# Kernel optimization log

Hardware: AMD Instinct MI355X
Metric: run time of the kernel (lower is better)

## Reference

```python
import jax, jax.numpy as jnp
import numpy as np

N = 384
C = 128     # pair_dim
H = 4       # num_head
D = C // H  # key/value dim per head = 32
LN_EPS = 1e-5


def setup_inputs() -> dict:
    key = jax.random.key(0)
    ks = jax.random.split(key, 12)
    s = 1.0 / np.sqrt(C)
    return {
        "pair_act": jax.random.normal(ks[0], (N, N, C), jnp.float32),
        "pair_mask": jax.random.randint(ks[1], (N, N), 0, 2, jnp.int32),
        "ln_scale": jax.random.uniform(ks[2], (C,), jnp.float32),
        "ln_bias": jax.random.normal(ks[3], (C,), jnp.float32) * 0.1,
        "feat_2d_weights": jax.random.normal(ks[4], (C, H), jnp.float32) * s,
        "q_w": jax.random.normal(ks[5], (C, H, D), jnp.float32) * s,
        "k_w": jax.random.normal(ks[6], (C, H, D), jnp.float32) * s,
        "v_w": jax.random.normal(ks[7], (C, H, D), jnp.float32) * s,
        "gating_w": jax.random.normal(ks[8], (C, H, D), jnp.float32) * s,
        "gating_b": jax.random.normal(ks[9], (H, D), jnp.float32) * 0.1,
        "o_w": jax.random.normal(ks[10], (H, D, C), jnp.float32) * s,
        "o_b": jax.random.normal(ks[11], (C,), jnp.float32) * 0.1,
    }


def reference(pair_act, pair_mask, ln_scale, ln_bias, feat_2d_weights,
              q_w, k_w, v_w, gating_w, gating_b, o_w, o_b):
    # orientation == 'per_row': no transpose
    # mask bias: [B, 1, 1, K]
    bias = (1e9 * (pair_mask.astype(pair_act.dtype) - 1.0))[:, None, None, :]
    # query_norm (LayerNorm over last dim)
    mu = jnp.mean(pair_act, axis=-1, keepdims=True)
    var = jnp.mean(jnp.square(pair_act - mu), axis=-1, keepdims=True)
    x = (pair_act - mu) * jax.lax.rsqrt(var + LN_EPS) * ln_scale + ln_bias
    # nonbatched pairwise bias per head: [H, Q, K]
    nb_bias = jnp.einsum('qkc,ch->hqk', x, feat_2d_weights)
    # AF2 gated attention (q_data = m_data = x)
    q = jnp.einsum('bqc,chd->bqhd', x, q_w) * (D ** -0.5)
    k = jnp.einsum('bkc,chd->bkhd', x, k_w)
    v = jnp.einsum('bkc,chd->bkhd', x, v_w)
    logits = jnp.einsum('bqhd,bkhd->bhqk', q, k) + bias + nb_bias[None]
    weights = jax.nn.softmax(logits, axis=-1)
    wavg = jnp.einsum('bhqk,bkhd->bqhd', weights, v)
    gate = jax.nn.sigmoid(jnp.einsum('bqc,chd->bqhd', x, gating_w) + gating_b)
    wavg = wavg * gate
    out = jnp.einsum('bqhd,hdc->bqc', wavg, o_w) + o_b
    return out
```

## Files before the change

### kernel.cpp

```cpp
#include <hip/hip_runtime.h>

typedef __bf16 bf16;
typedef __bf16 bf16x8 __attribute__((ext_vector_type(8)));
typedef __bf16 bf16x4v __attribute__((ext_vector_type(4)));
typedef short s16x4 __attribute__((ext_vector_type(4)));
typedef float f32x4 __attribute__((ext_vector_type(4)));
typedef unsigned int u32;
typedef unsigned long long u64;

#define NN 384
#define CC 128
#define LOG2E 1.44269504088896f

#define MFMA16(a,b,c) __builtin_amdgcn_mfma_f32_16x16x32_bf16(a,b,c,0,0,0)

#if __has_builtin(__builtin_amdgcn_mfma_f32_16x16x16_bf16)
typedef bf16x4v pvab_t;
static __device__ __forceinline__ f32x4 PVMFMA(pvab_t A, bf16x4v B, f32x4 C){
  return __builtin_amdgcn_mfma_f32_16x16x16_bf16(A, B, C, 0,0,0);
}
static __device__ __forceinline__ pvab_t mk_pvab(u32 w0, u32 w1){
  return __builtin_bit_cast(pvab_t, (u64)w0 | ((u64)w1<<32));
}
#else
typedef s16x4 pvab_t;
static __device__ __forceinline__ f32x4 PVMFMA(pvab_t A, bf16x4v B, f32x4 C){
  return __builtin_amdgcn_mfma_f32_16x16x16bf16_1k(A, __builtin_bit_cast(s16x4, B), C, 0,0,0);
}
static __device__ __forceinline__ pvab_t mk_pvab(u32 w0, u32 w1){
  return __builtin_bit_cast(pvab_t, (u64)w0 | ((u64)w1<<32));
}
#endif

static __device__ __forceinline__ u32 bpack(float a, float b){
  unsigned short x = __builtin_bit_cast(unsigned short, (bf16)a);
  unsigned short y = __builtin_bit_cast(unsigned short, (bf16)b);
  return (u32)x | ((u32)y<<16);
}

#define WS_NB   37748736
#define WS_QKVG 40108032
#define WS_OP   40239104
#define WS_KB   40271872
#define WS_VB   78020608
#define WS_NEED 115769344

__device__ __forceinline__ void async_copy16(void* lds_dst, const void* gsrc){
  __builtin_amdgcn_global_load_lds((const __attribute__((address_space(1))) u32*)gsrc,
                                   (__attribute__((address_space(3))) u32*)lds_dst, 16, 0, 0);
}

__global__ __launch_bounds__(256) void pack_kernel(
    const float* __restrict__ qw, const float* __restrict__ kw,
    const float* __restrict__ vw, const float* __restrict__ gw,
    const float* __restrict__ ow, bf16* __restrict__ qkvg, bf16* __restrict__ op)
{
  int tid = blockIdx.x*256 + threadIdx.x;
  int lane = tid & 63, frag = tid >> 6;
  if (frag < 128) {
    int f = frag & 1, t = (frag>>1)&3, h = (frag>>3)&3, wm = frag>>5;
    const float* W = wm==0?qw: (wm==1?kw: (wm==2?vw: gw));
    float sc = (wm==0) ? 0.17677669529663687f*LOG2E : (wm==3 ? LOG2E : 1.0f);
    int d = f*16 + (lane&15);
    #pragma unroll
    for (int j=0;j<8;j++){
      int c = t*32 + (lane>>4)*8 + j;
      qkvg[tid*8 + j] = (bf16)(W[c*128 + h*32 + d]*sc);
    }
  } else if (frag < 160) {
    int fr = frag - 128, f = fr & 7, t = fr>>3;
    int c = f*16 + (lane&15);
    #pragma unroll
    for (int j=0;j<8;j++){
      int d = (lane>>4)*8 + j;
      op[(fr*64 + lane)*8 + j] = (bf16)ow[(t*32 + d)*128 + c];
    }
  }
}

__global__ __launch_bounds__(256) void ln_kernel(
    const float* __restrict__ pa, const float* __restrict__ lns,
    const float* __restrict__ lnb, const float* __restrict__ fw,
    bf16* __restrict__ xout, float* __restrict__ nbout)
{
  int wid = (blockIdx.x*256 + threadIdx.x) >> 6;
  int lane = threadIdx.x & 63;
  int nw = (gridDim.x*256) >> 6;
  float2 sc = *(const float2*)(lns + lane*2);
  float2 bi = *(const float2*)(lnb + lane*2);
  float4 f0 = *(const float4*)(fw + lane*8);
  float4 f1 = *(const float4*)(fw + lane*8 + 4);
  for (int row = wid; row < NN*NN; row += nw){
    float2 v = *(const float2*)(pa + row*128 + lane*2);
    float s = v.x + v.y;
    float sq = v.x*v.x + v.y*v.y;
    #pragma unroll
    for (int m=1;m<64;m<<=1){ s += __shfl_xor(s,m); sq += __shfl_xor(sq,m); }
    float mu = s*(1.f/128.f);
    float rstd = rsqrtf(sq*(1.f/128.f) - mu*mu + 1e-5f);
    float x0 = (v.x-mu)*rstd*sc.x + bi.x;
    float x1 = (v.y-mu)*rstd*sc.y + bi.y;
    unsigned short h0 = __builtin_bit_cast(unsigned short, (bf16)x0);
    unsigned short h1 = __builtin_bit_cast(unsigned short, (bf16)x1);
    *(unsigned int*)((char*)xout + row*256 + lane*4) = ((unsigned int)h1<<16)|h0;
    float4 t;
    t.x = x0*f0.x + x1*f1.x;
    t.y = x0*f0.y + x1*f1.y;
    t.z = x0*f0.z + x1*f1.z;
    t.w = x0*f0.w + x1*f1.w;
    #pragma unroll
    for (int m=1;m<64;m<<=1){
      t.x += __shfl_xor(t.x,m); t.y += __shfl_xor(t.y,m);
      t.z += __shfl_xor(t.z,m); t.w += __shfl_xor(t.w,m);
    }
    float vsel = (lane==0)?t.x : (lane==1)?t.y : (lane==2)?t.z : t.w;
    if (lane < 4) nbout[(size_t)lane*(NN*NN) + row] = vsel*LOG2E;
  }
}

__global__ __launch_bounds__(256) void proj_kv_kernel(
    const bf16* __restrict__ xg, const bf16* __restrict__ qkvg,
    const int* __restrict__ mask, bf16* __restrict__ kbuf, bf16* __restrict__ vbuf)
{
  __shared__ char psm[16384];
  const int w = threadIdx.x>>6, lane = threadIdx.x&63, g = (lane>>4)&3, l15 = lane&15;
  const int W = blockIdx.x*4 + w;
  const int rt = W>>1, wm = 1 + (W&1);
  const f32x4 Z = {0.f,0.f,0.f,0.f};
  f32x4 acc[8];
  #pragma unroll
  for (int f8=0;f8<8;f8++) acc[f8] = Z;
  const bf16* xrow = xg + (size_t)(rt*16 + l15)*CC;
  #pragma unroll
  for (int t=0;t<4;t++){
    bf16x8 a = *(const bf16x8*)(xrow + t*32 + g*8);
    #pragma unroll
    for (int f8=0; f8<8; f8++){
      int h = f8>>1, fh = f8&1;
      bf16x8 bb = *(const bf16x8*)(qkvg + (((wm*4+h)*4+t)*2+fh)*512 + lane*8);
      acc[f8] = MFMA16(a, bb, acc[f8]);
    }
  }
  const int bq = rt/24, tau = rt%24;
  if (wm==1){
    char* scr = psm + w*4096;
    #pragma unroll
    for (int f8=0; f8<8; f8++){
      #pragma unroll
      for (int j=0;j<4;j++){
        unsigned r = g*4+j;
        *(bf16*)(scr + ((r*256 + (f8*16+l15)*2) ^ (((r>>1)&7)<<4))) = (bf16)acc[f8][j];
      }
    }
    #pragma unroll
    for (int h=0;h<4;h++){
      bf16x8 kf = *(const bf16x8*)(scr + ((l15*256 + h*64 + g*16) ^ (((l15>>1)&7)<<4)));
      *(bf16x8*)(kbuf + (((size_t)(bq*4+h)*24 + tau)*64 + lane)*8) = kf;
    }
  } else {
    int4 mi = *(const int4*)(mask + bq*NN + tau*16 + g*4);
    float mb[4] = { mi.x?1.f:0.f, mi.y?1.f:0.f, mi.z?1.f:0.f, mi.w?1.f:0.f };
    #pragma unroll
    for (int f8=0; f8<8; f8++){
      #pragma unroll
      for (int j=0;j<4;j++) acc[f8][j] *= mb[j];
    }
    #pragma unroll
    for (int h=0;h<4;h++){
      f32x4 a0 = acc[h*2+0], a1 = acc[h*2+1];
      uint4 st4;
      st4.x = bpack(a0[0], a0[1]);
      st4.y = bpack(a0[2], a0[3]);
      st4.z = bpack(a1[0], a1[1]);
      st4.w = bpack(a1[2], a1[3]);
      *(uint4*)((char*)vbuf + ((size_t)(bq*4+h)*24 + tau)*1024 + lane*16) = st4;
    }
  }
}

#define L14_SCR  49152
#define L14_MASK 53248
#define L14_TOT  54016

__global__ __attribute__((amdgpu_flat_work_group_size(256,256), amdgpu_waves_per_eu(2,4)))
void attn_kernel14(
    const bf16* __restrict__ xg, const int* __restrict__ mask,
    const float* __restrict__ nb, const bf16* __restrict__ qkvg,
    bf16* __restrict__ kbuf, const bf16* __restrict__ vbuf,
    const float* __restrict__ gb)
{
  __shared__ char sm[L14_TOT];
  const int tid = threadIdx.x;
  const int lane = tid & 63, w = tid >> 6;
  const int g = (lane >> 4)&3, l15 = lane & 15;
  const f32x4 Z = {0.f,0.f,0.f,0.f};

  const u32 bid = blockIdx.x;
  const int h = bid / 384;
  const int b = bid - h*384;

  const char* kbh = (const char*)kbuf + ((size_t)b*4 + h)*24576;
  const char* vbh = (const char*)vbuf + ((size_t)b*4 + h)*24576;

  #pragma unroll
  for (int i=0;i<6;i++){
    unsigned u = (i*4 + w)*1024;
    async_copy16(sm + u,         kbh + u + lane*16);
    async_copy16(sm + 24576 + u, vbh + u + lane*16);
  }
  for (int k = tid; k < NN; k += 256)
    *(bf16*)(sm + L14_MASK + k*2) = (bf16)(float)(mask[b*NN + k] != 0);
  __syncthreads();

  const unsigned scb = L14_SCR + w*1024;
  const float* nbh = nb + (size_t)h*(NN*NN);

  for (int i=0;i<6;i++){
    const int qt = w*6 + i;
    const int qb = qt*16;

    bf16x8 a4[4];
    #pragma unroll
    for (int t=0;t<4;t++)
      a4[t] = *(const bf16x8*)(xg + (size_t)(b*NN + qb + l15)*CC + t*32 + g*8);

    f32x4 q0=Z, q1=Z;
    #pragma unroll
    for (int t=0;t<4;t++){
      bf16x8 bq0 = *(const bf16x8*)(qkvg + (((0*4+h)*4+t)*2+0)*512 + lane*8);
      bf16x8 bq1 = *(const bf16x8*)(qkvg + (((0*4+h)*4+t)*2+1)*512 + lane*8);
      q0 = MFMA16(a4[t], bq0, q0);
      q1 = MFMA16(a4[t], bq1, q1);
    }
    #pragma unroll
    for (int f=0;f<2;f++){
      f32x4 qq = f ? q1 : q0;
      #pragma unroll
      for (int j=0;j<4;j++){
        unsigned r = g*4 + j, cb = (f*16 + l15)*2;
        *(bf16*)(sm + scb + ((r*64 + cb) ^ (((r>>1)&7)<<4))) = (bf16)qq[j];
      }
    }
    bf16x8 aq = *(const bf16x8*)(sm + scb + ((l15*64 + g*16) ^ (((l15>>1)&7)<<4)));

    f32x4 o0=Z, o1=Z, o2=Z;
    const float* nbq = nbh + (size_t)(qb + l15)*NN;

    #pragma unroll
    for (int c=0;c<6;c++){
      f32x4 st[4];
      #pragma unroll
      for (int nf=0;nf<4;nf++){
        float4 nbv = *(const float4*)(nbq + c*64 + nf*16 + g*4);
        bf16x8 ka = *(const bf16x8*)(sm + (c*4+nf)*1024 + lane*16);
        st[nf] = MFMA16(ka, aq, __builtin_bit_cast(f32x4, nbv));
      }
      #pragma unroll
      for (int nf=0;nf<4;nf++){
        #pragma unroll
        for (int j=0;j<4;j++)
          st[nf][j] = exp2f(st[nf][j] - 28.8539008178f);
      }
      #pragma unroll
      for (int nf=0;nf<4;nf++){
        pvab_t pa = mk_pvab(bpack(st[nf][0], st[nf][1]), bpack(st[nf][2], st[nf][3]));
        bf16x4v mk4 = *(const bf16x4v*)(sm + L14_MASK + (c*64 + nf*16 + g*4)*2);
        bf16x8 vv = *(const bf16x8*)(sm + 24576 + (c*4+nf)*1024 + lane*16);
        bf16x4v vlo = {vv[0],vv[1],vv[2],vv[3]};
        bf16x4v vhi = {vv[4],vv[5],vv[6],vv[7]};
        o0 = PVMFMA(pa, vlo, o0);
        o1 = PVMFMA(pa, vhi, o1);
        o2 = PVMFMA(pa, mk4, o2);
      }
    }

    float rcd[4];
    #pragma unroll
    for (int j=0;j<4;j++)
      rcd[j] = __builtin_amdgcn_rcpf(o2[j]);

    f32x4 g0=Z, g1=Z;
    #pragma unroll
    for (int t=0;t<4;t++){
      bf16x8 bg0 = *(const bf16x8*)(qkvg + (((3*4+h)*4+t)*2+0)*512 + lane*8);
      bf16x8 bg1 = *(const bf16x8*)(qkvg + (((3*4+h)*4+t)*2+1)*512 + lane*8);
      g0 = MFMA16(a4[t], bg0, g0);
      g1 = MFMA16(a4[t], bg1, g1);
    }

    #pragma unroll
    for (int f=0;f<2;f++){
      f32x4 ov = f ? o1 : o0, gv = f ? g1 : g0;
      int d = f*16 + l15;
      float gbv = gb[h*32 + d]*LOG2E;
      #pragma unroll
      for (int j=0;j<4;j++){
        float gt = 1.f/(1.f + exp2f(-(gv[j] + gbv)));
        float wg = ov[j]*rcd[j]*gt;
        unsigned r = g*4 + j, cb2 = (unsigned)d*2;
        *(bf16*)(sm + scb + ((r*64 + cb2) ^ (((r>>1)&7)<<4))) = (bf16)wg;
      }
    }
    bf16x8 awg = *(const bf16x8*)(sm + scb + ((l15*64 + g*16) ^ (((l15>>1)&7)<<4)));
    *(bf16x8*)((char*)kbuf + ((size_t)b*4 + h)*24576 + qt*1024 + lane*16) = awg;
  }
}

__global__ __launch_bounds__(256) void outproj_kernel(
    const bf16* __restrict__ wavg, const bf16* __restrict__ opk,
    const float* __restrict__ ob, float* __restrict__ out)
{
  const int w = threadIdx.x>>6, lane = threadIdx.x&63;
  const int g = (lane>>4)&3, l15 = lane&15;
  const f32x4 Z = {0.f,0.f,0.f,0.f};
  const int W = blockIdx.x*4 + w;
  const int b = W/24, qt = W%24, qb = qt*16;

  bf16x8 aw[4];
  #pragma unroll
  for (int h=0;h<4;h++)
    aw[h] = *(const bf16x8*)((const char*)wavg + ((size_t)b*4 + h)*24576 + qt*1024 + lane*16);

  f32x4 outa[8];
  #pragma unroll
  for (int nf=0;nf<8;nf++) outa[nf] = Z;
  #pragma unroll
  for (int h=0;h<4;h++){
    #pragma unroll
    for (int nf=0;nf<8;nf++){
      bf16x8 bo = *(const bf16x8*)(opk + ((h*8+nf)*64 + lane)*8);
      outa[nf] = MFMA16(aw[h], bo, outa[nf]);
    }
  }
  #pragma unroll
  for (int nf=0;nf<8;nf++){
    int c = nf*16 + l15;
    float obv = ob[c];
    #pragma unroll
    for (int j=0;j<4;j++){
      int qi = qb + g*4 + j;
      out[((size_t)b*NN + qi)*CC + c] = outa[nf][j] + obv;
    }
  }
}

extern "C" void kernel_launch(void* const* d_in, const int* in_sizes, int n_in,
                              void* d_out, int out_size, void* d_ws, size_t ws_size,
                              hipStream_t stream)
{
  (void)in_sizes; (void)n_in; (void)out_size; (void)ws_size;
  const float* pa  = (const float*)d_in[0];
  const int*   msk = (const int*)d_in[1];
  const float* lns = (const float*)d_in[2];
  const float* lnb = (const float*)d_in[3];
  const float* fw  = (const float*)d_in[4];
  const float* qw  = (const float*)d_in[5];
  const float* kw  = (const float*)d_in[6];
  const float* vw  = (const float*)d_in[7];
  const float* gw  = (const float*)d_in[8];
  const float* gbv = (const float*)d_in[9];
  const float* ow  = (const float*)d_in[10];
  const float* ob  = (const float*)d_in[11];
  float* out = (float*)d_out;

  char* ws = (char*)d_ws;
  bf16*  xbuf  = (bf16*)(ws);
  float* nbbuf = (float*)(ws + WS_NB);
  bf16*  qkvg  = (bf16*)(ws + WS_QKVG);
  bf16*  opk   = (bf16*)(ws + WS_OP);
  bf16*  kbuf  = (bf16*)(ws + WS_KB);
  bf16*  vbuf  = (bf16*)(ws + WS_VB);

  pack_kernel<<<40, 256, 0, stream>>>(qw, kw, vw, gw, ow, qkvg, opk);
  ln_kernel<<<1152, 256, 0, stream>>>(pa, lns, lnb, fw, xbuf, nbbuf);
  proj_kv_kernel<<<4608, 256, 0, stream>>>(xbuf, qkvg, msk, kbuf, vbuf);
  attn_kernel14<<<1536, 256, 0, stream>>>(xbuf, msk, nbbuf, qkvg, kbuf, vbuf, gbv);
  outproj_kernel<<<2304, 256, 0, stream>>>(kbuf, opk, ob, out);
}
```

Baseline: 322.7 us.

## Compute Q transposed in registers, use 16x16x16 QK MFMAs, move mask into exponent

The Q projection is computed transposed (weights as the A operand), so its output fragment feeds a pair of 16x16x16 MFMAs directly. This removes the LDS scratch write/read round trip for Q, and the K buffer layout is split into two halves to match. The mask becomes an additive -1e9*log2e bias inside the exponent, and the softmax denominator is a register sum with cross-lane shuffles instead of an extra mask MFMA. This trades one MFMA per tile for scalar adds and shuffles, and the QK step now issues twice as many smaller MFMAs.

```diff
diff --git a/kernel.cpp b/kernel.cpp
--- a/kernel.cpp
+++ b/kernel.cpp
@@ -19,18 +19,18 @@
 static __device__ __forceinline__ f32x4 PVMFMA(pvab_t A, bf16x4v B, f32x4 C){
   return __builtin_amdgcn_mfma_f32_16x16x16_bf16(A, B, C, 0,0,0);
 }
-static __device__ __forceinline__ pvab_t mk_pvab(u32 w0, u32 w1){
-  return __builtin_bit_cast(pvab_t, (u64)w0 | ((u64)w1<<32));
-}
 #else
 typedef s16x4 pvab_t;
 static __device__ __forceinline__ f32x4 PVMFMA(pvab_t A, bf16x4v B, f32x4 C){
   return __builtin_amdgcn_mfma_f32_16x16x16bf16_1k(A, __builtin_bit_cast(s16x4, B), C, 0,0,0);
 }
+#endif
 static __device__ __forceinline__ pvab_t mk_pvab(u32 w0, u32 w1){
   return __builtin_bit_cast(pvab_t, (u64)w0 | ((u64)w1<<32));
 }
-#endif
+static __device__ __forceinline__ pvab_t as_pvab(bf16x4v v){
+  return __builtin_bit_cast(pvab_t, v);
+}
 
 static __device__ __forceinline__ u32 bpack(float a, float b){
   unsigned short x = __builtin_bit_cast(unsigned short, (bf16)a);
@@ -154,8 +154,11 @@
     }
     #pragma unroll
     for (int h=0;h<4;h++){
-      bf16x8 kf = *(const bf16x8*)(scr + ((l15*256 + h*64 + g*16) ^ (((l15>>1)&7)<<4)));
-      *(bf16x8*)(kbuf + (((size_t)(bq*4+h)*24 + tau)*64 + lane)*8) = kf;
+      bf16x4v k0 = *(const bf16x4v*)(scr + ((l15*256 + h*64      + g*8) ^ (((l15>>1)&7)<<4)));
+      bf16x4v k1 = *(const bf16x4v*)(scr + ((l15*256 + h*64 + 32 + g*8) ^ (((l15>>1)&7)<<4)));
+      char* base = (char*)kbuf + (((size_t)(bq*4+h)*24 + tau)*1024);
+      *(bf16x4v*)(base +       lane*8) = k0;
+      *(bf16x4v*)(base + 512 + lane*8) = k1;
     }
   } else {
     int4 mi = *(const int4*)(mask + bq*NN + tau*16 + g*4);
@@ -178,18 +181,18 @@
   }
 }
 
-#define L14_SCR  49152
-#define L14_MASK 53248
-#define L14_TOT  54016
+#define L17_SCR  49152
+#define L17_MASK 53248
+#define L17_TOT  54016
 
 __global__ __attribute__((amdgpu_flat_work_group_size(256,256), amdgpu_waves_per_eu(2,4)))
-void attn_kernel14(
+void attn_kernel17(
     const bf16* __restrict__ xg, const int* __restrict__ mask,
     const float* __restrict__ nb, const bf16* __restrict__ qkvg,
     bf16* __restrict__ kbuf, const bf16* __restrict__ vbuf,
     const float* __restrict__ gb)
 {
-  __shared__ char sm[L14_TOT];
+  __shared__ char sm[L17_TOT];
   const int tid = threadIdx.x;
   const int lane = tid & 63, w = tid >> 6;
   const int g = (lane >> 4)&3, l15 = lane & 15;
@@ -209,10 +212,10 @@
     async_copy16(sm + 24576 + u, vbh + u + lane*16);
   }
   for (int k = tid; k < NN; k += 256)
-    *(bf16*)(sm + L14_MASK + k*2) = (bf16)(float)(mask[b*NN + k] != 0);
+    *(bf16*)(sm + L17_MASK + k*2) = (bf16)(1.44269504e9f*((float)mask[b*NN + k] - 1.0f));
   __syncthreads();
 
-  const unsigned scb = L14_SCR + w*1024;
+  const unsigned scb = L17_SCR + w*1024;
   const float* nbh = nb + (size_t)h*(NN*NN);
 
   for (int i=0;i<6;i++){
@@ -224,26 +227,19 @@
     for (int t=0;t<4;t++)
       a4[t] = *(const bf16x8*)(xg + (size_t)(b*NN + qb + l15)*CC + t*32 + g*8);
 
-    f32x4 q0=Z, q1=Z;
+    f32x4 Qt0=Z, Qt1=Z;
     #pragma unroll
     for (int t=0;t<4;t++){
-      bf16x8 bq0 = *(const bf16x8*)(qkvg + (((0*4+h)*4+t)*2+0)*512 + lane*8);
-      bf16x8 bq1 = *(const bf16x8*)(qkvg + (((0*4+h)*4+t)*2+1)*512 + lane*8);
-      q0 = MFMA16(a4[t], bq0, q0);
-      q1 = MFMA16(a4[t], bq1, q1);
-    }
-    #pragma unroll
-    for (int f=0;f<2;f++){
-      f32x4 qq = f ? q1 : q0;
-      #pragma unroll
-      for (int j=0;j<4;j++){
-        unsigned r = g*4 + j, cb = (f*16 + l15)*2;
-        *(bf16*)(sm + scb + ((r*64 + cb) ^ (((r>>1)&7)<<4))) = (bf16)qq[j];
-      }
-    }
-    bf16x8 aq = *(const bf16x8*)(sm + scb + ((l15*64 + g*16) ^ (((l15>>1)&7)<<4)));
-
-    f32x4 o0=Z, o1=Z, o2=Z;
+      bf16x8 wq0 = *(const bf16x8*)(qkvg + (((0*4+h)*4+t)*2+0)*512 + lane*8);
+      bf16x8 wq1 = *(const bf16x8*)(qkvg + (((0*4+h)*4+t)*2+1)*512 + lane*8);
+      Qt0 = MFMA16(wq0, a4[t], Qt0);
+      Qt1 = MFMA16(wq1, a4[t], Qt1);
+    }
+    bf16x4v qb0 = {(bf16)Qt0[0], (bf16)Qt0[1], (bf16)Qt0[2], (bf16)Qt0[3]};
+    bf16x4v qb1 = {(bf16)Qt1[0], (bf16)Qt1[1], (bf16)Qt1[2], (bf16)Qt1[3]};
+
+    float sum_ = 0.f;
+    f32x4 o0=Z, o1=Z;
     const float* nbq = nbh + (size_t)(qb + l15)*NN;
 
     #pragma unroll
@@ -252,32 +248,39 @@
       #pragma unroll
       for (int nf=0;nf<4;nf++){
         float4 nbv = *(const float4*)(nbq + c*64 + nf*16 + g*4);
-        bf16x8 ka = *(const bf16x8*)(sm + (c*4+nf)*1024 + lane*16);
-        st[nf] = MFMA16(ka, aq, __builtin_bit_cast(f32x4, nbv));
+        bf16x4v kA0 = *(const bf16x4v*)(sm + (c*4+nf)*1024 +       lane*8);
+        bf16x4v kA1 = *(const bf16x4v*)(sm + (c*4+nf)*1024 + 512 + lane*8);
+        f32x4 s0 = PVMFMA(as_pvab(kA0), qb0, __builtin_bit_cast(f32x4, nbv));
+        st[nf]   = PVMFMA(as_pvab(kA1), qb1, s0);
       }
       #pragma unroll
       for (int nf=0;nf<4;nf++){
+        bf16x4v mk4 = *(const bf16x4v*)(sm + L17_MASK + (c*64 + nf*16 + g*4)*2);
         #pragma unroll
-        for (int j=0;j<4;j++)
-          st[nf][j] = exp2f(st[nf][j] - 28.8539008178f);
+        for (int j=0;j<4;j++){
+          float pv = exp2f(st[nf][j] + (float)mk4[j] - 28.8539008178f);
+          st[nf][j] = pv;
+          sum_ += pv;
+        }
       }
       #pragma unroll
       for (int nf=0;nf<4;nf++){
         pvab_t pa = mk_pvab(bpack(st[nf][0], st[nf][1]), bpack(st[nf][2], st[nf][3]));
-        bf16x4v mk4 = *(const bf16x4v*)(sm + L14_MASK + (c*64 + nf*16 + g*4)*2);
         bf16x8 vv = *(const bf16x8*)(sm + 24576 + (c*4+nf)*1024 + lane*16);
         bf16x4v vlo = {vv[0],vv[1],vv[2],vv[3]};
         bf16x4v vhi = {vv[4],vv[5],vv[6],vv[7]};
         o0 = PVMFMA(pa, vlo, o0);
         o1 = PVMFMA(pa, vhi, o1);
-        o2 = PVMFMA(pa, mk4, o2);
-      }
-    }
-
+      }
+    }
+
+    sum_ += __shfl_xor(sum_, 16);
+    sum_ += __shfl_xor(sum_, 32);
+    float rsl = 1.f/sum_;
     float rcd[4];
     #pragma unroll
     for (int j=0;j<4;j++)
-      rcd[j] = __builtin_amdgcn_rcpf(o2[j]);
+      rcd[j] = __shfl(rsl, (lane & 0x30) + g*4 + j);
 
     f32x4 g0=Z, g1=Z;
     #pragma unroll
@@ -374,6 +377,6 @@
   pack_kernel<<<40, 256, 0, stream>>>(qw, kw, vw, gw, ow, qkvg, opk);
   ln_kernel<<<1152, 256, 0, stream>>>(pa, lns, lnb, fw, xbuf, nbbuf);
   proj_kv_kernel<<<4608, 256, 0, stream>>>(xbuf, qkvg, msk, kbuf, vbuf);
-  attn_kernel14<<<1536, 256, 0, stream>>>(xbuf, msk, nbbuf, qkvg, kbuf, vbuf, gbv);
+  attn_kernel17<<<1536, 256, 0, stream>>>(xbuf, msk, nbbuf, qkvg, kbuf, vbuf, gbv);
   outproj_kernel<<<2304, 256, 0, stream>>>(kbuf, opk, ob, out);
 }
```

Result: slower. 334.1 us (+3.5%).

## Process two query tiles per iteration and apply mask as additive logit bias

Applied to the files above, without the earlier changes.

The attention kernel now handles two 16-row query tiles per loop iteration, so each K/V fragment loaded from LDS feeds two MFMAs instead of one. The mask becomes an additive bias (scaled by log2e·1e9) added before exp2, which replaces the third PV MFMA that used to accumulate the softmax denominator. The row sum is instead accumulated in registers and reduced with lane shuffles. Register pressure roughly doubles per wave, which can lower occupancy. Masked-out entries now rely on exp2 underflowing to zero rather than being multiplied by zero.

```diff
diff --git a/kernel.cpp b/kernel.cpp
--- a/kernel.cpp
+++ b/kernel.cpp
@@ -19,18 +19,15 @@
 static __device__ __forceinline__ f32x4 PVMFMA(pvab_t A, bf16x4v B, f32x4 C){
   return __builtin_amdgcn_mfma_f32_16x16x16_bf16(A, B, C, 0,0,0);
 }
-static __device__ __forceinline__ pvab_t mk_pvab(u32 w0, u32 w1){
-  return __builtin_bit_cast(pvab_t, (u64)w0 | ((u64)w1<<32));
-}
 #else
 typedef s16x4 pvab_t;
 static __device__ __forceinline__ f32x4 PVMFMA(pvab_t A, bf16x4v B, f32x4 C){
   return __builtin_amdgcn_mfma_f32_16x16x16bf16_1k(A, __builtin_bit_cast(s16x4, B), C, 0,0,0);
 }
+#endif
 static __device__ __forceinline__ pvab_t mk_pvab(u32 w0, u32 w1){
   return __builtin_bit_cast(pvab_t, (u64)w0 | ((u64)w1<<32));
 }
-#endif
 
 static __device__ __forceinline__ u32 bpack(float a, float b){
   unsigned short x = __builtin_bit_cast(unsigned short, (bf16)a);
@@ -178,18 +175,18 @@
   }
 }
 
-#define L14_SCR  49152
-#define L14_MASK 53248
-#define L14_TOT  54016
+#define L18_SCR  49152
+#define L18_MASK 57344
+#define L18_TOT  58112
 
 __global__ __attribute__((amdgpu_flat_work_group_size(256,256), amdgpu_waves_per_eu(2,4)))
-void attn_kernel14(
+void attn_kernel18(
     const bf16* __restrict__ xg, const int* __restrict__ mask,
     const float* __restrict__ nb, const bf16* __restrict__ qkvg,
     bf16* __restrict__ kbuf, const bf16* __restrict__ vbuf,
     const float* __restrict__ gb)
 {
-  __shared__ char sm[L14_TOT];
+  __shared__ char sm[L18_TOT];
   const int tid = threadIdx.x;
   const int lane = tid & 63, w = tid >> 6;
   const int g = (lane >> 4)&3, l15 = lane & 15;
@@ -209,100 +206,132 @@
     async_copy16(sm + 24576 + u, vbh + u + lane*16);
   }
   for (int k = tid; k < NN; k += 256)
-    *(bf16*)(sm + L14_MASK + k*2) = (bf16)(float)(mask[b*NN + k] != 0);
+    *(bf16*)(sm + L18_MASK + k*2) = (bf16)(1.44269504e9f*((float)mask[b*NN + k] - 1.0f));
   __syncthreads();
 
-  const unsigned scb = L14_SCR + w*1024;
+  const unsigned scbA = L18_SCR + w*2048;
+  const unsigned scbB = scbA + 1024;
   const float* nbh = nb + (size_t)h*(NN*NN);
 
-  for (int i=0;i<6;i++){
-    const int qt = w*6 + i;
-    const int qb = qt*16;
-
-    bf16x8 a4[4];
-    #pragma unroll
-    for (int t=0;t<4;t++)
-      a4[t] = *(const bf16x8*)(xg + (size_t)(b*NN + qb + l15)*CC + t*32 + g*8);
-
-    f32x4 q0=Z, q1=Z;
+  for (int i=0;i<3;i++){
+    const int qtA = w*6 + i*2, qtB = qtA + 1;
+    const int qbA = qtA*16,    qbB = qtB*16;
+
+    bf16x8 a4A[4], a4B[4];
+    #pragma unroll
+    for (int t=0;t<4;t++){
+      a4A[t] = *(const bf16x8*)(xg + (size_t)(b*NN + qbA + l15)*CC + t*32 + g*8);
+      a4B[t] = *(const bf16x8*)(xg + (size_t)(b*NN + qbB + l15)*CC + t*32 + g*8);
+    }
+
+    f32x4 qA0=Z, qA1=Z, qB0=Z, qB1=Z;
     #pragma unroll
     for (int t=0;t<4;t++){
       bf16x8 bq0 = *(const bf16x8*)(qkvg + (((0*4+h)*4+t)*2+0)*512 + lane*8);
       bf16x8 bq1 = *(const bf16x8*)(qkvg + (((0*4+h)*4+t)*2+1)*512 + lane*8);
-      q0 = MFMA16(a4[t], bq0, q0);
-      q1 = MFMA16(a4[t], bq1, q1);
+      qA0 = MFMA16(a4A[t], bq0, qA0);
+      qA1 = MFMA16(a4A[t], bq1, qA1);
+      qB0 = MFMA16(a4B[t], bq0, qB0);
+      qB1 = MFMA16(a4B[t], bq1, qB1);
     }
     #pragma unroll
     for (int f=0;f<2;f++){
-      f32x4 qq = f ? q1 : q0;
+      f32x4 qqA = f ? qA1 : qA0, qqB = f ? qB1 : qB0;
       #pragma unroll
       for (int j=0;j<4;j++){
         unsigned r = g*4 + j, cb = (f*16 + l15)*2;
-        *(bf16*)(sm + scb + ((r*64 + cb) ^ (((r>>1)&7)<<4))) = (bf16)qq[j];
-      }
-    }
-    bf16x8 aq = *(const bf16x8*)(sm + scb + ((l15*64 + g*16) ^ (((l15>>1)&7)<<4)));
-
-    f32x4 o0=Z, o1=Z, o2=Z;
-    const float* nbq = nbh + (size_t)(qb + l15)*NN;
+        unsigned off = (r*64 + cb) ^ (((r>>1)&7)<<4);
+        *(bf16*)(sm + scbA + off) = (bf16)qqA[j];
+        *(bf16*)(sm + scbB + off) = (bf16)qqB[j];
+      }
+    }
+    unsigned aqoff = (l15*64 + g*16) ^ (((l15>>1)&7)<<4);
+    bf16x8 aqA = *(const bf16x8*)(sm + scbA + aqoff);
+    bf16x8 aqB = *(const bf16x8*)(sm + scbB + aqoff);
+
+    float sumA = 0.f, sumB = 0.f;
+    f32x4 oA0=Z, oA1=Z, oB0=Z, oB1=Z;
+    const float* nbqA = nbh + (size_t)(qbA + l15)*NN;
+    const float* nbqB = nbh + (size_t)(qbB + l15)*NN;
 
     #pragma unroll
     for (int c=0;c<6;c++){
-      f32x4 st[4];
+      f32x4 stA[4], stB[4];
       #pragma unroll
       for (int nf=0;nf<4;nf++){
-        float4 nbv = *(const float4*)(nbq + c*64 + nf*16 + g*4);
         bf16x8 ka = *(const bf16x8*)(sm + (c*4+nf)*1024 + lane*16);
-        st[nf] = MFMA16(ka, aq, __builtin_bit_cast(f32x4, nbv));
+        float4 nbvA = *(const float4*)(nbqA + c*64 + nf*16 + g*4);
+        float4 nbvB = *(const float4*)(nbqB + c*64 + nf*16 + g*4);
+        stA[nf] = MFMA16(ka, aqA, __builtin_bit_cast(f32x4, nbvA));
+        stB[nf] = MFMA16(ka, aqB, __builtin_bit_cast(f32x4, nbvB));
       }
       #pragma unroll
       for (int nf=0;nf<4;nf++){
+        bf16x4v mk4 = *(const bf16x4v*)(sm + L18_MASK + (c*64 + nf*16 + g*4)*2);
         #pragma unroll
-        for (int j=0;j<4;j++)
-          st[nf][j] = exp2f(st[nf][j] - 28.8539008178f);
+        for (int j=0;j<4;j++){
+          float pvA = exp2f(stA[nf][j] + (float)mk4[j] - 28.8539008178f);
+          float pvB = exp2f(stB[nf][j] + (float)mk4[j] - 28.8539008178f);
+          stA[nf][j] = pvA; sumA += pvA;
+          stB[nf][j] = pvB; sumB += pvB;
+        }
       }
       #pragma unroll
       for (int nf=0;nf<4;nf++){
-        pvab_t pa = mk_pvab(bpack(st[nf][0], st[nf][1]), bpack(st[nf][2], st[nf][3]));
-        bf16x4v mk4 = *(const bf16x4v*)(sm + L14_MASK + (c*64 + nf*16 + g*4)*2);
         bf16x8 vv = *(const bf16x8*)(sm + 24576 + (c*4+nf)*1024 + lane*16);
         bf16x4v vlo = {vv[0],vv[1],vv[2],vv[3]};
         bf16x4v vhi = {vv[4],vv[5],vv[6],vv[7]};
-        o0 = PVMFMA(pa, vlo, o0);
-        o1 = PVMFMA(pa, vhi, o1);
-        o2 = PVMFMA(pa, mk4, o2);
-      }
-    }
-
-    float rcd[4];
-    #pragma unroll
-    for (int j=0;j<4;j++)
-      rcd[j] = __builtin_amdgcn_rcpf(o2[j]);
-
-    f32x4 g0=Z, g1=Z;
+        pvab_t paA = mk_pvab(bpack(stA[nf][0], stA[nf][1]), bpack(stA[nf][2], stA[nf][3]));
+        pvab_t paB = mk_pvab(bpack(stB[nf][0], stB[nf][1]), bpack(stB[nf][2], stB[nf][3]));
+        oA0 = PVMFMA(paA, vlo, oA0);
+        oB0 = PVMFMA(paB, vlo, oB0);
+        oA1 = PVMFMA(paA, vhi, oA1);
+        oB1 = PVMFMA(paB, vhi, oB1);
+      }
+    }
+
+    sumA += __shfl_xor(sumA, 16); sumA += __shfl_xor(sumA, 32);
+    sumB += __shfl_xor(sumB, 16); sumB += __shfl_xor(sumB, 32);
+    float rslA = 1.f/sumA, rslB = 1.f/sumB;
+    float rcdA[4], rcdB[4];
+    #pragma unroll
+    for (int j=0;j<4;j++){
+      int src = (lane & 0x30) + g*4 + j;
+      rcdA[j] = __shfl(rslA, src);
+      rcdB[j] = __shfl(rslB, src);
+    }
+
+    f32x4 gA0=Z, gA1=Z, gB0=Z, gB1=Z;
     #pragma unroll
     for (int t=0;t<4;t++){
       bf16x8 bg0 = *(const bf16x8*)(qkvg + (((3*4+h)*4+t)*2+0)*512 + lane*8);
       bf16x8 bg1 = *(const bf16x8*)(qkvg + (((3*4+h)*4+t)*2+1)*512 + lane*8);
-      g0 = MFMA16(a4[t], bg0, g0);
-      g1 = MFMA16(a4[t], bg1, g1);
+      gA0 = MFMA16(a4A[t], bg0, gA0);
+      gA1 = MFMA16(a4A[t], bg1, gA1);
+      gB0 = MFMA16(a4B[t], bg0, gB0);
+      gB1 = MFMA16(a4B[t], bg1, gB1);
     }
 
     #pragma unroll
     for (int f=0;f<2;f++){
-      f32x4 ov = f ? o1 : o0, gv = f ? g1 : g0;
+      f32x4 ovA = f ? oA1 : oA0, gvA = f ? gA1 : gA0;
+      f32x4 ovB = f ? oB1 : oB0, gvB = f ? gB1 : gB0;
       int d = f*16 + l15;
       float gbv = gb[h*32 + d]*LOG2E;
       #pragma unroll
       for (int j=0;j<4;j++){
-        float gt = 1.f/(1.f + exp2f(-(gv[j] + gbv)));
-        float wg = ov[j]*rcd[j]*gt;
         unsigned r = g*4 + j, cb2 = (unsigned)d*2;
-        *(bf16*)(sm + scb + ((r*64 + cb2) ^ (((r>>1)&7)<<4))) = (bf16)wg;
-      }
-    }
-    bf16x8 awg = *(const bf16x8*)(sm + scb + ((l15*64 + g*16) ^ (((l15>>1)&7)<<4)));
-    *(bf16x8*)((char*)kbuf + ((size_t)b*4 + h)*24576 + qt*1024 + lane*16) = awg;
+        unsigned off = (r*64 + cb2) ^ (((r>>1)&7)<<4);
+        float gtA = 1.f/(1.f + exp2f(-(gvA[j] + gbv)));
+        float gtB = 1.f/(1.f + exp2f(-(gvB[j] + gbv)));
+        *(bf16*)(sm + scbA + off) = (bf16)(ovA[j]*rcdA[j]*gtA);
+        *(bf16*)(sm + scbB + off) = (bf16)(ovB[j]*rcdB[j]*gtB);
+      }
+    }
+    bf16x8 awgA = *(const bf16x8*)(sm + scbA + aqoff);
+    bf16x8 awgB = *(const bf16x8*)(sm + scbB + aqoff);
+    *(bf16x8*)((char*)kbuf + ((size_t)b*4 + h)*24576 + qtA*1024 + lane*16) = awgA;
+    *(bf16x8*)((char*)kbuf + ((size_t)b*4 + h)*24576 + qtB*1024 + lane*16) = awgB;
   }
 }
 
@@ -374,6 +403,6 @@
   pack_kernel<<<40, 256, 0, stream>>>(qw, kw, vw, gw, ow, qkvg, opk);
   ln_kernel<<<1152, 256, 0, stream>>>(pa, lns, lnb, fw, xbuf, nbbuf);
   proj_kv_kernel<<<4608, 256, 0, stream>>>(xbuf, qkvg, msk, kbuf, vbuf);
-  attn_kernel14<<<1536, 256, 0, stream>>>(xbuf, msk, nbbuf, qkvg, kbuf, vbuf, gbv);
+  attn_kernel18<<<1536, 256, 0, stream>>>(xbuf, msk, nbbuf, qkvg, kbuf, vbuf, gbv);
   outproj_kernel<<<2304, 256, 0, stream>>>(kbuf, opk, ob, out);
 }
```

Measured after the change: 295.6 us. 8.4% less time.
